# Optimization experiments

Hardware: AMD Instinct MI355X
Metric: run time of the kernel (lower is better)

Reference implementation:

```python
import jax, jax.numpy as jnp
import numpy as np


def setup_inputs() -> dict:
    key = jax.random.key(0)
    k1, k2, k3 = jax.random.split(key, 3)
    B, T, F, H = 4, 2048, 256, 8
    x = jax.random.normal(k1, (B, T, F), dtype=jnp.float32)
    W_qkv = jax.random.normal(k2, (F, H * F * 3), dtype=jnp.float32) * (1.0 / np.sqrt(F))
    b_qkv = jnp.zeros((H * F * 3,), dtype=jnp.float32)
    W_proj = jax.random.normal(k3, (H * F, F), dtype=jnp.float32) * (1.0 / np.sqrt(H * F))
    b_proj = jnp.zeros((F,), dtype=jnp.float32)
    return {"x": x, "W_qkv": W_qkv, "b_qkv": b_qkv, "W_proj": W_proj, "b_proj": b_proj}


def reference(x, W_qkv, b_qkv, W_proj, b_proj):
    # x: [B, T, F]; heads H = 8, per-head dim = F (full in_features per head)
    B, T, F = x.shape
    H = W_qkv.shape[1] // (F * 3)
    temperature = 1.0
    qkv = x @ W_qkv + b_qkv                      # [B, T, H*F*3]
    qkv = qkv.reshape(B, T, H, F, 3)
    qkv = jnp.transpose(qkv, (0, 2, 1, 3, 4))    # [B, H, T, F, 3]
    inv_sqrt_f = 1.0 / jnp.sqrt(jnp.asarray(F, x.dtype))
    q = qkv[..., 0] * inv_sqrt_f                 # note: BOTH q and k scaled
    k = qkv[..., 1] * inv_sqrt_f
    v = qkv[..., 2]
    scores = jnp.einsum('bhtf,bhsf->bhts', q, k) / temperature  # [B, H, T, T]
    weights = jax.nn.softmax(scores, axis=-1)
    out = jnp.einsum('bhts,bhsf->bhtf', weights, v)              # [B, H, T, F]
    out = jnp.transpose(out, (0, 2, 1, 3)).reshape(B, T, H * F)  # [B, T, H*F]
    return out @ W_proj + b_proj                                 # [B, T, F]
```

## Files before the change

kernel.cpp:

```cpp
#include <hip/hip_runtime.h>
#include <hip/hip_bf16.h>


typedef __attribute__((ext_vector_type(8))) short bf16x8;
typedef __attribute__((ext_vector_type(4))) short s16x4;
typedef __attribute__((ext_vector_type(4))) float f32x4;
typedef __attribute__((ext_vector_type(16))) float f32x16;
typedef __attribute__((ext_vector_type(4))) int i32x4;

#define MFMA16(a, b, c) __builtin_amdgcn_mfma_f32_16x16x32_bf16((a), (b), (c), 0, 0, 0)
#define MFMA32(a, b, c) __builtin_amdgcn_mfma_f32_32x32x16_bf16((a), (b), (c), 0, 0, 0)

static __device__ __forceinline__ short bf16_bits(float v) {
    __hip_bfloat16 h = __float2bfloat16(v);
    return reinterpret_cast<short&>(h);
}

static __device__ __forceinline__ unsigned pack_bf16(float lo, float hi) {
    unsigned a = (unsigned)(unsigned short)bf16_bits(lo);
    unsigned b = (unsigned)(unsigned short)bf16_bits(hi);
    return a | (b << 16);
}

static __device__ __forceinline__ void dma_lds16(const void* g, void* l) {
    __builtin_amdgcn_global_load_lds((const __attribute__((address_space(1))) unsigned int*)g,
                                     (__attribute__((address_space(3))) unsigned int*)l,
                                     16, 0, 0);
}

static __device__ __forceinline__ i32x4 cvt8(const float* __restrict__ src) {
    f32x4 a = *(const f32x4*)(src);
    f32x4 b = *(const f32x4*)(src + 4);
    union { short s[8]; i32x4 v; } u;
#pragma unroll
    for (int i = 0; i < 4; ++i) {
        u.s[i]     = bf16_bits(a[i]);
        u.s[i + 4] = bf16_bits(b[i]);
    }
    return u.v;
}

__global__ __launch_bounds__(256) void k_pre(const float* __restrict__ x,
                                             const float* __restrict__ W_qkv,
                                             const float* __restrict__ W_proj,
                                             __hip_bfloat16* __restrict__ Xb,
                                             __hip_bfloat16* __restrict__ WqkvT,
                                             __hip_bfloat16* __restrict__ WprojT) {
    const int id = blockIdx.x;
    if (id < 1024) {
        size_t i = ((size_t)id * 256 + threadIdx.x) * 8;
        *(i32x4*)(Xb + i) = cvt8(x + i);
        return;
    }
    __shared__ __hip_bfloat16 tile[32][33];
    const int tx = threadIdx.x & 31;
    const int ty = threadIdx.x >> 5;
    if (id < 2560) {
        const int t = id - 1024;
        const int c0 = (t % 192) * 32, r0 = (t / 192) * 32;
#pragma unroll
        for (int j = 0; j < 4; ++j)
            tile[ty + j * 8][tx] =
                __float2bfloat16(W_qkv[(size_t)(r0 + ty + j * 8) * 6144 + c0 + tx]);
        __syncthreads();
#pragma unroll
        for (int j = 0; j < 4; ++j) {
            int n = c0 + ty + j * 8;
            int h = n / 768, rem = n - h * 768;
            int f = rem / 3, c = rem - f * 3;
            int np = c * 2048 + h * 256 + f;
            WqkvT[(size_t)np * 256 + r0 + tx] = tile[tx][ty + j * 8];
        }
    } else {
        const int t = id - 2560;
        const int c0 = (t & 7) * 32, r0 = (t >> 3) * 32;
#pragma unroll
        for (int j = 0; j < 4; ++j)
            tile[ty + j * 8][tx] =
                __float2bfloat16(W_proj[(size_t)(r0 + ty + j * 8) * 256 + c0 + tx]);
        __syncthreads();
#pragma unroll
        for (int j = 0; j < 4; ++j)
            WprojT[(size_t)(c0 + ty + j * 8) * 2048 + r0 + tx] = tile[tx][ty + j * 8];
    }
}

#define GS 32
__global__ __launch_bounds__(256) void k_gemm_qkv(const __hip_bfloat16* __restrict__ X,
                                                  const __hip_bfloat16* __restrict__ Wt,
                                                  const float* __restrict__ bias,
                                                  __hip_bfloat16* __restrict__ Q,
                                                  __hip_bfloat16* __restrict__ K,
                                                  __hip_bfloat16* __restrict__ Vt) {
    __shared__ __align__(16) short As[2][128 * GS];
    __shared__ __align__(16) short Bs[2][128 * GS];
    const int tid = threadIdx.x;
    const int m0 = blockIdx.y * 128, n0 = blockIdx.x * 128;
    const int w = tid >> 6, lane = tid & 63, l16 = lane & 15, quad = lane >> 4;
    const int wm = (w >> 1) * 64, wn = (w & 1) * 64;

    const int ci0 = (w * 2 + 0) * 64 + lane, ci1 = (w * 2 + 1) * 64 + lane;
    const int r0s = ci0 >> 2, c0s = (ci0 & 3) * 8;
    const int r1s = ci1 >> 2, c1s = (ci1 & 3) * 8;

    f32x4 acc[4][4];
#pragma unroll
    for (int mi = 0; mi < 4; ++mi)
#pragma unroll
        for (int ni = 0; ni < 4; ++ni) acc[mi][ni] = (f32x4){0.f, 0.f, 0.f, 0.f};

    dma_lds16(X + (size_t)(m0 + r0s) * 256 + c0s, &As[0][(w * 2 + 0) * 512]);
    dma_lds16(Wt + (size_t)(n0 + r0s) * 256 + c0s, &Bs[0][(w * 2 + 0) * 512]);
    dma_lds16(X + (size_t)(m0 + r1s) * 256 + c1s, &As[0][(w * 2 + 1) * 512]);
    dma_lds16(Wt + (size_t)(n0 + r1s) * 256 + c1s, &Bs[0][(w * 2 + 1) * 512]);

    for (int it = 0; it < 8; ++it) {
        const int cur = it & 1, nxt = cur ^ 1;
        if (it < 7) {
            const int k0 = (it + 1) * 32;
            dma_lds16(X + (size_t)(m0 + r0s) * 256 + k0 + c0s, &As[nxt][(w * 2 + 0) * 512]);
            dma_lds16(Wt + (size_t)(n0 + r0s) * 256 + k0 + c0s, &Bs[nxt][(w * 2 + 0) * 512]);
            dma_lds16(X + (size_t)(m0 + r1s) * 256 + k0 + c1s, &As[nxt][(w * 2 + 1) * 512]);
            dma_lds16(Wt + (size_t)(n0 + r1s) * 256 + k0 + c1s, &Bs[nxt][(w * 2 + 1) * 512]);
            asm volatile("s_waitcnt vmcnt(4)" ::: "memory");
        } else {
            asm volatile("s_waitcnt vmcnt(0)" ::: "memory");
        }
        __builtin_amdgcn_s_barrier();

        bf16x8 af[4], bfr[4];
#pragma unroll
        for (int mi = 0; mi < 4; ++mi)
            af[mi] = *(const bf16x8*)&As[cur][(wm + mi * 16 + l16) * GS + quad * 8];
#pragma unroll
        for (int ni = 0; ni < 4; ++ni)
            bfr[ni] = *(const bf16x8*)&Bs[cur][(wn + ni * 16 + l16) * GS + quad * 8];
#pragma unroll
        for (int mi = 0; mi < 4; ++mi)
#pragma unroll
            for (int ni = 0; ni < 4; ++ni)
                acc[mi][ni] = MFMA16(af[mi], bfr[ni], acc[mi][ni]);

        asm volatile("s_waitcnt lgkmcnt(0)" ::: "memory");
        __builtin_amdgcn_s_barrier();
    }

    const int c = n0 >> 11;
    if (c < 2) {
        __hip_bfloat16* dst = (c == 0) ? Q : K;
        const int h = ((n0 + wn) >> 8) & 7;
        const int fb = (n0 + wn) & 255;
        const int m_base = m0 + wm;
        const int b = m_base >> 11;
        short* ebuf = &As[0][0] + w * (16 * 68);
#pragma unroll
        for (int mi = 0; mi < 4; ++mi) {
#pragma unroll
            for (int ni = 0; ni < 4; ++ni) {
                float bv = bias[h * 768 + (fb + ni * 16 + l16) * 3 + c];
#pragma unroll
                for (int r = 0; r < 4; ++r)
                    ebuf[(quad * 4 + r) * 68 + ni * 16 + l16] =
                        bf16_bits((acc[mi][ni][r] + bv) * 0.0625f);
            }
            asm volatile("s_waitcnt lgkmcnt(0)" ::: "memory");
#pragma unroll
            for (int p = 0; p < 2; ++p) {
                int row = p * 8 + (lane >> 3), cc = lane & 7;
                i32x4 v = *(const i32x4*)&ebuf[row * 68 + cc * 8];
                int t = (m_base + mi * 16 + row) & 2047;
                *(i32x4*)(dst + ((size_t)(b * 8 + h) * 2048 + t) * 256 + fb + cc * 8) = v;
            }
            asm volatile("s_waitcnt lgkmcnt(0)" ::: "memory");
        }
    } else {
        const int pos = ((quad & 1) << 3) | ((quad >> 1) << 2);
#pragma unroll
        for (int mi = 0; mi < 4; ++mi) {
            int m = m0 + wm + mi * 16 + quad * 4;
            int b = m >> 11, t = m & 2047;
            size_t tcol = (size_t)(t & ~31) + ((mi & 1) << 4) + pos;
#pragma unroll
            for (int ni = 0; ni < 4; ++ni) {
                int np = n0 + wn + ni * 16 + l16;
                int h = (np >> 8) & 7, f = np & 255;
                float bv = bias[h * 768 + f * 3 + 2];
                s16x4 v;
#pragma unroll
                for (int r = 0; r < 4; ++r) v[r] = bf16_bits(acc[mi][ni][r] + bv);
                *(s16x4*)(Vt + ((size_t)(b * 8 + h) * 256 + f) * 2048 + tcol) = v;
            }
        }
    }
}

#define VSS 40
#define ES 40
__global__ __launch_bounds__(512) void k_flash(const __hip_bfloat16* __restrict__ Q,
                                               const __hip_bfloat16* __restrict__ K,
                                               const __hip_bfloat16* __restrict__ Vt,
                                               __hip_bfloat16* __restrict__ O) {
    __shared__ __align__(16) short Ks[2][32 * 256];
    __shared__ __align__(16) short Vs[2][256 * VSS];
    const int tid = threadIdx.x;
    const int w = tid >> 6, lane = tid & 63;
    const int l32 = lane & 31, hi = lane >> 5;

    const int id = blockIdx.x;
    const int slot = id >> 3;
    const int bh = (id & 7) * 4 + (slot & 3);
    const int q0 = (slot >> 2) * 256;

    const __hip_bfloat16* Qb = Q + (size_t)bh * 2048 * 256;
    const __hip_bfloat16* Kb = K + (size_t)bh * 2048 * 256;
    const __hip_bfloat16* Vb = Vt + (size_t)bh * 256 * 2048;

    bf16x8 qf[16];
    {
        const __hip_bfloat16* qrow_p = Qb + (size_t)(q0 + w * 32 + l32) * 256 + hi * 8;
#pragma unroll
        for (int kf = 0; kf < 16; ++kf) qf[kf] = *(const bf16x8*)(qrow_p + kf * 16);
    }

    f32x16 oacc[8];
#pragma unroll
    for (int nt = 0; nt < 8; ++nt)
#pragma unroll
        for (int r = 0; r < 16; ++r) oacc[nt][r] = 0.f;
    float lsum = 0.f;

    const int vrow = (tid >> 2);
    const int vcol = (tid & 3) * 8;

#pragma unroll
    for (int p = 0; p < 2; ++p) {
        int seg = w * 2 + p;
        int r = 2 * seg + hi;
        int clog = l32 ^ (r & 7);
        dma_lds16(Kb + (size_t)r * 256 + clog * 8, &Ks[0][seg * 512]);
    }
#pragma unroll
    for (int p = 0; p < 2; ++p) {
        int row = vrow + p * 128;
        *(i32x4*)&Vs[0][row * VSS + vcol] = *(const i32x4*)(Vb + (size_t)row * 2048 + vcol);
    }
    __syncthreads();

    const int s7 = l32 & 7;
    for (int it = 0; it < 64; ++it) {
        const int cur = it & 1, nxt = cur ^ 1;
        const bool more = it < 63;
        const int ktn = (it + 1) * 32;

        i32x4 vreg[2];
        if (more) {
#pragma unroll
            for (int p = 0; p < 2; ++p) {
                int seg = w * 2 + p;
                int r = 2 * seg + hi;
                int clog = l32 ^ (r & 7);
                dma_lds16(Kb + (size_t)(ktn + r) * 256 + clog * 8, &Ks[nxt][seg * 512]);
            }
#pragma unroll
            for (int p = 0; p < 2; ++p) {
                int row = vrow + p * 128;
                vreg[p] = *(const i32x4*)(Vb + (size_t)row * 2048 + ktn + vcol);
            }
        }

        f32x16 s;
#pragma unroll
        for (int r = 0; r < 16; ++r) s[r] = 0.f;
        const short* ksb = &Ks[cur][l32 * 256];
#pragma unroll
        for (int kf = 0; kf < 16; ++kf) {
            int g = kf * 2 + hi;
            bf16x8 kfr = *(const bf16x8*)&ksb[((g ^ s7) * 8)];
            s = MFMA32(kfr, qf[kf], s);
        }

#pragma unroll
        for (int kk = 0; kk < 2; ++kk) {
            unsigned ch[4];
#pragma unroll
            for (int c = 0; c < 4; ++c) {
                float e0 = __expf(s[8 * kk + 2 * c]);
                float e1 = __expf(s[8 * kk + 2 * c + 1]);
                lsum += e0 + e1;
                ch[c] = pack_bf16(e0, e1);
            }
            union { i32x4 i; bf16x8 v; } pf;
            pf.i = (i32x4){(int)ch[0], (int)ch[1], (int)ch[2], (int)ch[3]};

#pragma unroll
            for (int nt = 0; nt < 8; ++nt) {
                bf16x8 vf = *(const bf16x8*)&Vs[cur][(nt * 32 + l32) * VSS + kk * 16 + hi * 8];
                oacc[nt] = MFMA32(vf, pf.v, oacc[nt]);
            }
        }

        if (more) {
#pragma unroll
            for (int p = 0; p < 2; ++p) {
                int row = vrow + p * 128;
                *(i32x4*)&Vs[nxt][row * VSS + vcol] = vreg[p];
            }
        }
        __syncthreads();
    }

    lsum += __shfl_xor(lsum, 32);
    const float inv = 1.f / lsum;

    short* ebuf = &Ks[0][0] + w * (32 * ES);
    const int b = bh >> 3, hh = bh & 7;
#pragma unroll
    for (int nt = 0; nt < 8; ++nt) {
#pragma unroll
        for (int r = 0; r < 16; ++r) {
            int fl = (r & 3) + 8 * (r >> 2) + 4 * hi;
            ebuf[l32 * ES + fl] = bf16_bits(oacc[nt][r] * inv);
        }
        asm volatile("s_waitcnt lgkmcnt(0)" ::: "memory");
#pragma unroll
        for (int p = 0; p < 2; ++p) {
            i32x4 v = *(const i32x4*)&ebuf[(lane >> 1) * ES + (lane & 1) * 8 + p * 16];
            int t = q0 + w * 32 + (lane >> 1);
            __hip_bfloat16* dst =
                O + ((size_t)(b * 2048 + t) * 2048 + hh * 256 + nt * 32 + (lane & 1) * 8 + p * 16);
            *(i32x4*)dst = v;
        }
        asm volatile("s_waitcnt lgkmcnt(0)" ::: "memory");
    }
}

__global__ __launch_bounds__(256) void k_gemm_proj(const __hip_bfloat16* __restrict__ A,
                                                   const __hip_bfloat16* __restrict__ Wt,
                                                   const float* __restrict__ bias,
                                                   float* __restrict__ Out) {
    __shared__ __align__(16) short As[2][64 * GS];
    __shared__ __align__(16) short Bs[2][64 * GS];
    const int tid = threadIdx.x;
    const int id = blockIdx.x;
    const int slot = id >> 3;
    const int n0 = (slot & 3) * 64;
    const int m0 = ((id & 7) + 8 * (slot >> 2)) * 64;
    const int w = tid >> 6, lane = tid & 63, l16 = lane & 15, quad = lane >> 4;
    const int wm = w * 16;

    const int rS = tid >> 2, cS = (tid & 3) * 8;

    f32x4 acc[4];
#pragma unroll
    for (int ni = 0; ni < 4; ++ni) acc[ni] = (f32x4){0.f, 0.f, 0.f, 0.f};

    dma_lds16(A + (size_t)(m0 + rS) * 2048 + cS, &As[0][w * 512]);
    dma_lds16(Wt + (size_t)(n0 + rS) * 2048 + cS, &Bs[0][w * 512]);

    for (int it = 0; it < 64; ++it) {
        const int cur = it & 1, nxt = cur ^ 1;
        if (it < 63) {
            const int k0 = (it + 1) * 32;
            dma_lds16(A + (size_t)(m0 + rS) * 2048 + k0 + cS, &As[nxt][w * 512]);
            dma_lds16(Wt + (size_t)(n0 + rS) * 2048 + k0 + cS, &Bs[nxt][w * 512]);
            asm volatile("s_waitcnt vmcnt(2)" ::: "memory");
        } else {
            asm volatile("s_waitcnt vmcnt(0)" ::: "memory");
        }
        __builtin_amdgcn_s_barrier();

        bf16x8 af = *(const bf16x8*)&As[cur][(wm + l16) * GS + quad * 8];
        bf16x8 bfr[4];
#pragma unroll
        for (int ni = 0; ni < 4; ++ni)
            bfr[ni] = *(const bf16x8*)&Bs[cur][(ni * 16 + l16) * GS + quad * 8];
#pragma unroll
        for (int ni = 0; ni < 4; ++ni)
            acc[ni] = MFMA16(af, bfr[ni], acc[ni]);

        asm volatile("s_waitcnt lgkmcnt(0)" ::: "memory");
        __builtin_amdgcn_s_barrier();
    }

#pragma unroll
    for (int ni = 0; ni < 4; ++ni) {
        int n = n0 + ni * 16 + l16;
        float bv = bias[n];
#pragma unroll
        for (int r = 0; r < 4; ++r) {
            int m = m0 + wm + quad * 4 + r;
            Out[(size_t)m * 256 + n] = acc[ni][r] + bv;
        }
    }
}

extern "C" void kernel_launch(void* const* d_in, const int* in_sizes, int n_in,
                              void* d_out, int out_size, void* d_ws, size_t ws_size,
                              hipStream_t stream) {
    const float* x      = (const float*)d_in[0];
    const float* W_qkv  = (const float*)d_in[1];
    const float* b_qkv  = (const float*)d_in[2];
    const float* W_proj = (const float*)d_in[3];
    const float* b_proj = (const float*)d_in[4];
    float* out = (float*)d_out;

    const size_t E = 32ull * 2048 * 256;
    __hip_bfloat16* Qb     = (__hip_bfloat16*)d_ws;
    __hip_bfloat16* Kb     = Qb + E;
    __hip_bfloat16* Vt     = Kb + E;
    __hip_bfloat16* attn   = Vt + E;
    __hip_bfloat16* WqkvT  = attn + E;
    __hip_bfloat16* WprojT = WqkvT + 6144 * 256;
    __hip_bfloat16* Xb     = attn;

    k_pre<<<dim3(3072), 256, 0, stream>>>(x, W_qkv, W_proj, Xb, WqkvT, WprojT);
    k_gemm_qkv<<<dim3(48, 64), 256, 0, stream>>>(Xb, WqkvT, b_qkv, Qb, Kb, Vt);
    k_flash<<<dim3(256), 512, 0, stream>>>(Qb, Kb, Vt, attn);
    k_gemm_proj<<<dim3(512), 256, 0, stream>>>(attn, WprojT, b_proj, out);
}
```

Measured before the change: 290.3 us.

## Store V in MFMA-fragment order and read it directly from global in flash

The QKV GEMM now writes V in a tiled layout of 32-token by 32-feature fragments that matches the MFMA operand order. The flash kernel can then load V fragments straight from global memory instead of staging them through LDS with register double-buffering. This removes the V LDS buffers and their stores, and adds a launch-bounds hint for two blocks per CU. The QKV GEMM grid is also remapped to 1D with XCD-aware block assignment for better L2 locality. The risk is that per-iteration global V loads sit on the critical path with no prefetch, and every wave in a block rereads the same V data.

```diff
diff --git a/kernel.cpp b/kernel.cpp
--- a/kernel.cpp
+++ b/kernel.cpp
@@ -95,7 +95,13 @@
     __shared__ __align__(16) short As[2][128 * GS];
     __shared__ __align__(16) short Bs[2][128 * GS];
     const int tid = threadIdx.x;
-    const int m0 = blockIdx.y * 128, n0 = blockIdx.x * 128;
+    const int id = blockIdx.x;
+    const int xcd = id & 7;
+    const int local = id >> 3;
+    const int jn = local % 6;
+    const int mb = local / 6;
+    const int n0 = (xcd * 6 + jn) * 128;
+    const int m0 = mb * 128;
     const int w = tid >> 6, lane = tid & 63, l16 = lane & 15, quad = lane >> 4;
     const int wm = (w >> 1) * 64, wn = (w & 1) * 64;
 
@@ -174,12 +180,12 @@
             asm volatile("s_waitcnt lgkmcnt(0)" ::: "memory");
         }
     } else {
-        const int pos = ((quad & 1) << 3) | ((quad >> 1) << 2);
+        const int hib = quad & 1, jb = (quad >> 1) * 4;
 #pragma unroll
         for (int mi = 0; mi < 4; ++mi) {
             int m = m0 + wm + mi * 16 + quad * 4;
             int b = m >> 11, t = m & 2047;
-            size_t tcol = (size_t)(t & ~31) + ((mi & 1) << 4) + pos;
+            size_t base_t = (size_t)(t >> 5) * 8192 + (size_t)(((mi & 1) * 2 + hib) * 8) * 256 + jb;
 #pragma unroll
             for (int ni = 0; ni < 4; ++ni) {
                 int np = n0 + wn + ni * 16 + l16;
@@ -188,20 +194,19 @@
                 s16x4 v;
 #pragma unroll
                 for (int r = 0; r < 4; ++r) v[r] = bf16_bits(acc[mi][ni][r] + bv);
-                *(s16x4*)(Vt + ((size_t)(b * 8 + h) * 256 + f) * 2048 + tcol) = v;
-            }
-        }
-    }
-}
-
-#define VSS 40
+                *(s16x4*)((short*)Vt + (size_t)(b * 8 + h) * 524288 + base_t +
+                          (f >> 5) * 256 + (f & 31) * 8) = v;
+            }
+        }
+    }
+}
+
 #define ES 40
-__global__ __launch_bounds__(512) void k_flash(const __hip_bfloat16* __restrict__ Q,
-                                               const __hip_bfloat16* __restrict__ K,
-                                               const __hip_bfloat16* __restrict__ Vt,
-                                               __hip_bfloat16* __restrict__ O) {
+__global__ __launch_bounds__(512, 2) void k_flash(const __hip_bfloat16* __restrict__ Q,
+                                                  const __hip_bfloat16* __restrict__ K,
+                                                  const __hip_bfloat16* __restrict__ Vt,
+                                                  __hip_bfloat16* __restrict__ O) {
     __shared__ __align__(16) short Ks[2][32 * 256];
-    __shared__ __align__(16) short Vs[2][256 * VSS];
     const int tid = threadIdx.x;
     const int w = tid >> 6, lane = tid & 63;
     const int l32 = lane & 31, hi = lane >> 5;
@@ -213,7 +218,7 @@
 
     const __hip_bfloat16* Qb = Q + (size_t)bh * 2048 * 256;
     const __hip_bfloat16* Kb = K + (size_t)bh * 2048 * 256;
-    const __hip_bfloat16* Vb = Vt + (size_t)bh * 256 * 2048;
+    const short* Vb = (const short*)Vt + (size_t)bh * 524288;
 
     bf16x8 qf[16];
     {
@@ -228,9 +233,6 @@
 #pragma unroll
         for (int r = 0; r < 16; ++r) oacc[nt][r] = 0.f;
     float lsum = 0.f;
-
-    const int vrow = (tid >> 2);
-    const int vcol = (tid & 3) * 8;
 
 #pragma unroll
     for (int p = 0; p < 2; ++p) {
@@ -239,11 +241,6 @@
         int clog = l32 ^ (r & 7);
         dma_lds16(Kb + (size_t)r * 256 + clog * 8, &Ks[0][seg * 512]);
     }
-#pragma unroll
-    for (int p = 0; p < 2; ++p) {
-        int row = vrow + p * 128;
-        *(i32x4*)&Vs[0][row * VSS + vcol] = *(const i32x4*)(Vb + (size_t)row * 2048 + vcol);
-    }
     __syncthreads();
 
     const int s7 = l32 & 7;
@@ -252,7 +249,6 @@
         const bool more = it < 63;
         const int ktn = (it + 1) * 32;
 
-        i32x4 vreg[2];
         if (more) {
 #pragma unroll
             for (int p = 0; p < 2; ++p) {
@@ -261,11 +257,6 @@
                 int clog = l32 ^ (r & 7);
                 dma_lds16(Kb + (size_t)(ktn + r) * 256 + clog * 8, &Ks[nxt][seg * 512]);
             }
-#pragma unroll
-            for (int p = 0; p < 2; ++p) {
-                int row = vrow + p * 128;
-                vreg[p] = *(const i32x4*)(Vb + (size_t)row * 2048 + ktn + vcol);
-            }
         }
 
         f32x16 s;
@@ -279,6 +270,7 @@
             s = MFMA32(kfr, qf[kf], s);
         }
 
+        const short* Vit = Vb + (size_t)it * 8192 + hi * 2048 + l32 * 8;
 #pragma unroll
         for (int kk = 0; kk < 2; ++kk) {
             unsigned ch[4];
@@ -294,18 +286,11 @@
 
 #pragma unroll
             for (int nt = 0; nt < 8; ++nt) {
-                bf16x8 vf = *(const bf16x8*)&Vs[cur][(nt * 32 + l32) * VSS + kk * 16 + hi * 8];
+                bf16x8 vf = *(const bf16x8*)(Vit + kk * 4096 + nt * 256);
                 oacc[nt] = MFMA32(vf, pf.v, oacc[nt]);
             }
         }
 
-        if (more) {
-#pragma unroll
-            for (int p = 0; p < 2; ++p) {
-                int row = vrow + p * 128;
-                *(i32x4*)&Vs[nxt][row * VSS + vcol] = vreg[p];
-            }
-        }
         __syncthreads();
     }
 
@@ -414,7 +399,7 @@
     __hip_bfloat16* Xb     = attn;
 
     k_pre<<<dim3(3072), 256, 0, stream>>>(x, W_qkv, W_proj, Xb, WqkvT, WprojT);
-    k_gemm_qkv<<<dim3(48, 64), 256, 0, stream>>>(Xb, WqkvT, b_qkv, Qb, Kb, Vt);
+    k_gemm_qkv<<<dim3(3072), 256, 0, stream>>>(Xb, WqkvT, b_qkv, Qb, Kb, Vt);
     k_flash<<<dim3(256), 512, 0, stream>>>(Qb, Kb, Vt, attn);
     k_gemm_proj<<<dim3(512), 256, 0, stream>>>(attn, WprojT, b_proj, out);
 }
```

Result: slower. 334.5 us (+15.2%).
